# Optimization experiments

Measured on AMD Instinct MI355X. Metric: run time of the kernel, lower is better.

Reference implementation:

```python
import jax, jax.numpy as jnp
import numpy as np

B, T, D = 4, 1024, 2048
H = 32
HD = D // H  # 64
NEG = -1e9


def setup_inputs() -> dict:
    key = jax.random.key(0)
    ks = jax.random.split(key, 12)
    s = 0.02
    x = jax.random.normal(ks[0], (B, T, D), dtype=jnp.float32)
    # additive causal mask [1, 1, T, T]
    causal = jnp.tril(jnp.ones((T, T), dtype=bool))
    attention_mask = jnp.where(causal, 0.0, NEG).astype(jnp.float32)[None, None]
    cache = jnp.zeros((B, 2, T, H, HD), dtype=jnp.float32)
    return {
        "x": x,
        "attention_mask": attention_mask,
        "cache": cache,
        "cache_update_index": 0,
        "Wq": jax.random.normal(ks[1], (D, D), jnp.float32) * s,
        "bq": jnp.zeros((D,), jnp.float32),
        "Wk": jax.random.normal(ks[2], (D, D), jnp.float32) * s,
        "bk": jnp.zeros((D,), jnp.float32),
        "Wv": jax.random.normal(ks[3], (D, D), jnp.float32) * s,
        "bv": jnp.zeros((D,), jnp.float32),
        "Wo": jax.random.normal(ks[4], (D, D), jnp.float32) * s,
        "bo": jnp.zeros((D,), jnp.float32),
    }


def _split_heads(t):
    b, s, _ = t.shape
    return t.reshape(b, s, H, HD).transpose(0, 2, 1, 3)  # (B,H,T,HD)


def reference(x, attention_mask, cache, cache_update_index, Wq, bq, Wk, bk, Wv, bv, Wo, bo):
    q = _split_heads(x @ Wq + bq)  # (B,H,T,HD)
    k = _split_heads(x @ Wk + bk)
    v = _split_heads(x @ Wv + bv)

    # update KV cache (cache layout: [B, 2, max_len, H, HD])
    k_for_cache = k.transpose(0, 2, 1, 3)  # (B,T,H,HD)
    v_for_cache = v.transpose(0, 2, 1, 3)
    idx = (0, cache_update_index, 0, 0)
    k_cache = jax.lax.dynamic_update_slice(cache[:, 0], k_for_cache, idx)
    v_cache = jax.lax.dynamic_update_slice(cache[:, 1], v_for_cache, idx)
    new_cache = jnp.stack([k_cache, v_cache], axis=1)
    k = k_cache.transpose(0, 2, 1, 3)  # (B,H,S,HD)
    v = v_cache.transpose(0, 2, 1, 3)

    scale = jnp.asarray(HD, q.dtype) ** -0.5
    scores = jnp.einsum("bhqd,bhkd->bhqk", q, k) * scale + attention_mask.astype(q.dtype)
    attn = jax.nn.softmax(scores, axis=-1)
    ctx = jnp.einsum("bhqk,bhkd->bhqd", attn, v)  # (B,H,T,HD)
    merged = ctx.transpose(0, 2, 1, 3).reshape(x.shape[0], x.shape[1], D)
    out = merged @ Wo + bo
    return out, new_cache
```

## Files before the change

kernel.cpp:

```cpp
#include <hip/hip_runtime.h>
#include <hip/hip_bf16.h>
#include <stdint.h>


typedef __hip_bfloat16 bf16;
typedef unsigned short us;
typedef short s16x8 __attribute__((ext_vector_type(8)));
typedef float f32x4 __attribute__((ext_vector_type(4)));

#define T_SEQ   1024
#define D_MODEL 2048

__device__ inline us f2b(float f) {
    bf16 h = __float2bfloat16(f);
    return *(us*)&h;
}

typedef __attribute__((address_space(1))) const void gas_void;
typedef __attribute__((address_space(3))) void las_void;

__device__ inline void gl2lds16(const void* g, void* l) {
    __builtin_amdgcn_global_load_lds((gas_void*)g, (las_void*)l, 16, 0, 0);
}

__global__ __launch_bounds__(256)
void cvtx_kernel(const float* __restrict__ x, us* __restrict__ xb)
{
    const size_t i = ((size_t)blockIdx.x * 256 + threadIdx.x) * 8;
    float4 a = *(const float4*)(x + i);
    float4 b = *(const float4*)(x + i + 4);
    union { uint4 u; us s[8]; } p;
    p.s[0] = f2b(a.x); p.s[1] = f2b(a.y); p.s[2] = f2b(a.z); p.s[3] = f2b(a.w);
    p.s[4] = f2b(b.x); p.s[5] = f2b(b.y); p.s[6] = f2b(b.z); p.s[7] = f2b(b.w);
    *(uint4*)(xb + i) = p.u;
}

__global__ __launch_bounds__(256)
void wtrans_kernel(const float* __restrict__ W0, const float* __restrict__ W1,
                   const float* __restrict__ W2, us* __restrict__ Wt)
{
    __shared__ float tile[64][65];
    const int z = blockIdx.z;
    const float* W = (z == 0) ? W0 : (z == 1) ? W1 : W2;
    us* dst = Wt + (size_t)z * D_MODEL * D_MODEL;

    const int tid = threadIdx.x;
    const int k0 = blockIdx.y * 64, n0 = blockIdx.x * 64;

    const int rr = tid >> 4, cc = (tid & 15) * 4;
    #pragma unroll
    for (int i = 0; i < 4; ++i) {
        float4 v = *(const float4*)(W + (size_t)(k0 + rr + i * 16) * D_MODEL + n0 + cc);
        tile[rr + i * 16][cc]     = v.x;
        tile[rr + i * 16][cc + 1] = v.y;
        tile[rr + i * 16][cc + 2] = v.z;
        tile[rr + i * 16][cc + 3] = v.w;
    }
    __syncthreads();

    const int nr = tid >> 3, kc = (tid & 7) * 8;
    #pragma unroll
    for (int i = 0; i < 2; ++i) {
        const int n = nr + i * 32;
        union { uint4 u; us s[8]; } p;
        #pragma unroll
        for (int j = 0; j < 8; ++j) p.s[j] = f2b(tile[kc + j][n]);
        *(uint4*)(dst + (size_t)(n0 + n) * D_MODEL + k0 + kc) = p.u;
    }
}

__global__ __launch_bounds__(256)
void v2t_kernel(const float* __restrict__ cache, us* __restrict__ vbt)
{
    __shared__ float tile[64][65];
    const int t0 = blockIdx.x * 64;
    const int h  = blockIdx.y;
    const int b  = blockIdx.z;

    const float* src = cache + ((size_t)(b * 2 + 1) * T_SEQ) * D_MODEL + h * 64;

    const int tid = threadIdx.x;
    const int rr = tid >> 4, cc = (tid & 15) * 4;
    #pragma unroll
    for (int i = 0; i < 4; ++i) {
        float4 v = *(const float4*)(src + (size_t)(t0 + rr + i * 16) * D_MODEL + cc);
        tile[rr + i * 16][cc]     = v.x;
        tile[rr + i * 16][cc + 1] = v.y;
        tile[rr + i * 16][cc + 2] = v.z;
        tile[rr + i * 16][cc + 3] = v.w;
    }
    __syncthreads();

    const int dr = tid >> 3, tc = (tid & 7) * 8;
    #pragma unroll
    for (int i = 0; i < 2; ++i) {
        const int d = dr + i * 32;
        union { uint4 u; us s[8]; } p;
        #pragma unroll
        for (int j = 0; j < 8; ++j) p.s[j] = f2b(tile[tc + j][d]);
        *(uint4*)(vbt + (size_t)((b * 32 + h) * 64 + d) * 1024 + t0 + tc) = p.u;
    }
}

template<int MODE>
__global__ __launch_bounds__(256, 3)
void gemm128_kernel(const us* __restrict__ A, const us* __restrict__ Bt,
                    const float* __restrict__ b0, const float* __restrict__ b1,
                    const float* __restrict__ b2,
                    float* __restrict__ out0, float* __restrict__ out1,
                    const int* __restrict__ idxp)
{
    __shared__ __align__(16) us As[128 * 64];
    __shared__ __align__(16) us Bs[128 * 64];

    const int tid  = threadIdx.x;
    const int wv   = tid >> 6;
    const int lane = tid & 63;
    const int quad = lane >> 4;
    const int l15  = lane & 15;
    const int wm   = wv >> 1;
    const int wn   = wv & 1;

    const int gx  = gridDim.x;
    const int nwg = gx * gridDim.y;
    int bid = blockIdx.y * gx + blockIdx.x;
    bid = (bid & 7) * (nwg >> 3) + (bid >> 3);
    const int m0 = (bid / gx) * 128;
    const int n0 = (bid % gx) * 128;

    const int srow = lane >> 3;
    const int scol = ((lane & 7) ^ srow) * 8;
    const us* aG = A  + (size_t)(m0 + wv * 32 + srow) * D_MODEL + scol;
    const us* bG = Bt + (size_t)(n0 + wv * 32 + srow) * D_MODEL + scol;
    us* aL = As + wv * 32 * 64;
    us* bL = Bs + wv * 32 * 64;

    f32x4 acc[4][4];
    #pragma unroll
    for (int mi = 0; mi < 4; ++mi)
        #pragma unroll
        for (int ni = 0; ni < 4; ++ni) acc[mi][ni] = f32x4{0.f, 0.f, 0.f, 0.f};

    const int xr = l15 & 7;
    #define LDA(MI, KK) (*(const s16x8*)(As + (wm * 64 + (MI) * 16 + l15) * 64 \
                          + ((((KK) * 4 + quad) ^ xr) * 8)))
    #define LDB(NI, KK) (*(const s16x8*)(Bs + (wn * 64 + (NI) * 16 + l15) * 64 \
                          + ((((KK) * 4 + quad) ^ xr) * 8)))

    for (int k0 = 0; k0 < D_MODEL; k0 += 64) {
        #pragma unroll
        for (int g = 0; g < 4; ++g) {
            gl2lds16(aG + k0 + g * 8 * D_MODEL, aL + g * 512);
            gl2lds16(bG + k0 + g * 8 * D_MODEL, bL + g * 512);
        }
        __syncthreads();

        #pragma unroll
        for (int kk = 0; kk < 2; ++kk) {
            s16x8 af[4], bfr[4];
            #pragma unroll
            for (int mi = 0; mi < 4; ++mi) af[mi] = LDA(mi, kk);
            #pragma unroll
            for (int ni = 0; ni < 4; ++ni) bfr[ni] = LDB(ni, kk);
            #pragma unroll
            for (int mi = 0; mi < 4; ++mi)
                #pragma unroll
                for (int ni = 0; ni < 4; ++ni)
                    acc[mi][ni] = __builtin_amdgcn_mfma_f32_16x16x32_bf16(
                        af[mi], bfr[ni], acc[mi][ni], 0, 0, 0);
        }
        __syncthreads();
    }
    #undef LDA
    #undef LDB

    const int seg = (MODE == 3) ? (n0 >> 11) : 0;
    const float* bias = (MODE == 3) ? (seg == 0 ? b0 : (seg == 1 ? b1 : b2)) : b0;
    const int idx = (MODE == 3 && seg > 0) ? idxp[0] : 0;

    #pragma unroll
    for (int ni = 0; ni < 4; ++ni) {
        const int col = n0 + wn * 64 + ni * 16 + l15;
        const int cl  = col & (D_MODEL - 1);
        const float bv = bias[cl];
        #pragma unroll
        for (int mi = 0; mi < 4; ++mi) {
            #pragma unroll
            for (int r = 0; r < 4; ++r) {
                const int m = m0 + wm * 64 + mi * 16 + quad * 4 + r;
                const float v = acc[mi][ni][r] + bv;
                if (MODE == 0) {
                    out0[(size_t)m * D_MODEL + cl] = v;
                } else {
                    if (seg == 0) {
                        ((us*)out0)[(size_t)m * D_MODEL + cl] = f2b(v * 0.125f);
                    } else {
                        const int b  = m >> 10;
                        const int tt = ((m & 1023) + idx) & 1023;
                        out1[((size_t)(b * 2 + (seg - 1)) * T_SEQ + tt) * D_MODEL + cl] = v;
                    }
                }
            }
        }
    }
}

#define LDW 72

__global__ __launch_bounds__(512, 4)
void attn_mfma_kernel(const us* __restrict__ q, const float* __restrict__ cache,
                      const us* __restrict__ vbt, us* __restrict__ ctx)
{
    __shared__ __align__(16) us Qs[128 * LDW];
    __shared__ __align__(16) us Ks[2][64 * LDW];
    __shared__ __align__(16) us Vt[2][64 * 64];

    const int tid  = threadIdx.x;
    const int wave = tid >> 6;
    const int lane = tid & 63;
    const int quad = lane >> 4;
    const int l15  = lane & 15;
    const int xr   = l15 & 7;

    const int bh = blockIdx.x;
    const int b  = bh >> 5;
    const int h  = bh & 31;
    const int qt = 7 - blockIdx.y;

    const float* kbase = cache + ((size_t)(b * 2 + 0) * T_SEQ) * D_MODEL + h * 64;
    const us* vb_bh = vbt + (size_t)((b * 32 + h) * 64) * 1024;

    {
        const int qrow = tid >> 2;
        const int qp   = tid & 3;
        const uint4* qg = (const uint4*)(q + (size_t)(b * T_SEQ + qt * 128 + qrow) * D_MODEL
                                           + h * 64 + qp * 16);
        uint4 q0 = qg[0], q1 = qg[1];
        *(uint4*)(Qs + qrow * LDW + qp * 16)     = q0;
        *(uint4*)(Qs + qrow * LDW + qp * 16 + 8) = q1;
    }

    const int ksrow = tid >> 3;
    const int kp8   = tid & 7;
    const int vrow  = lane >> 3;
    const int vchk  = (lane & 7) ^ vrow;
    const us* vG = vb_bh + (size_t)(wave * 8 + vrow) * 1024 + vchk * 8;

    const int nkt = 2 * qt + 2;

    gl2lds16(vG, (us*)Vt[0] + wave * 512);
    {
        const float4* kg = (const float4*)(kbase + (size_t)ksrow * D_MODEL + kp8 * 8);
        float4 k0 = kg[0], k1 = kg[1];
        union { uint4 u; us s[8]; } p;
        p.s[0] = f2b(k0.x); p.s[1] = f2b(k0.y); p.s[2] = f2b(k0.z); p.s[3] = f2b(k0.w);
        p.s[4] = f2b(k1.x); p.s[5] = f2b(k1.y); p.s[6] = f2b(k1.z); p.s[7] = f2b(k1.w);
        *(uint4*)(&Ks[0][ksrow * LDW + kp8 * 8]) = p.u;
    }
    __syncthreads();

    const s16x8 qf0 = *(const s16x8*)(Qs + (wave * 16 + l15) * LDW + quad * 8);
    const s16x8 qf1 = *(const s16x8*)(Qs + (wave * 16 + l15) * LDW + 32 + quad * 8);

    f32x4 oacc[4];
    #pragma unroll
    for (int t = 0; t < 4; ++t) oacc[t] = f32x4{0.f, 0.f, 0.f, 0.f};
    float m_run[4] = {-1e30f, -1e30f, -1e30f, -1e30f};
    float l_run[4] = {0.f, 0.f, 0.f, 0.f};

    for (int kt = 0; kt < nkt; ++kt) {
        const int buf = kt & 1;
        const bool more = (kt + 1 < nkt);

        float4 nk0, nk1;
        if (more) {
            gl2lds16(vG + (kt + 1) * 64, (us*)Vt[buf ^ 1] + wave * 512);
            const float4* kg = (const float4*)(kbase
                + (size_t)((kt + 1) * 64 + ksrow) * D_MODEL + kp8 * 8);
            nk0 = kg[0]; nk1 = kg[1];
        }

        const int kbr = kt * 64 - qt * 128;
        if (kbr < wave * 16 + 16) {
            const us* kb_ = Ks[buf];
            const us* vb_ = (const us*)Vt[buf];

            f32x4 sacc[4];
            #pragma unroll
            for (int t = 0; t < 4; ++t) sacc[t] = f32x4{0.f, 0.f, 0.f, 0.f};
            #pragma unroll
            for (int t = 0; t < 4; ++t) {
                s16x8 kf0 = *(const s16x8*)(kb_ + (t * 16 + l15) * LDW + quad * 8);
                s16x8 kf1 = *(const s16x8*)(kb_ + (t * 16 + l15) * LDW + 32 + quad * 8);
                sacc[t] = __builtin_amdgcn_mfma_f32_16x16x32_bf16(qf0, kf0, sacc[t], 0, 0, 0);
                sacc[t] = __builtin_amdgcn_mfma_f32_16x16x32_bf16(qf1, kf1, sacc[t], 0, 0, 0);
            }

            if (kbr + 63 > wave * 16) {
                #pragma unroll
                for (int t = 0; t < 4; ++t) {
                    const int keyl = kbr + t * 16 + l15;
                    #pragma unroll
                    for (int r = 0; r < 4; ++r) {
                        if (keyl > wave * 16 + quad * 4 + r) sacc[t][r] = -1e30f;
                    }
                }
            }

            float rmax[4];
            #pragma unroll
            for (int r = 0; r < 4; ++r)
                rmax[r] = fmaxf(fmaxf(sacc[0][r], sacc[1][r]), fmaxf(sacc[2][r], sacc[3][r]));
            #pragma unroll
            for (int off = 1; off < 16; off <<= 1) {
                #pragma unroll
                for (int r = 0; r < 4; ++r) rmax[r] = fmaxf(rmax[r], __shfl_xor(rmax[r], off, 16));
            }
            float alpha[4];
            #pragma unroll
            for (int r = 0; r < 4; ++r) {
                const float mnew = fmaxf(m_run[r], rmax[r]);
                alpha[r] = __expf(m_run[r] - mnew);
                m_run[r] = mnew;
            }
            float rsum[4] = {0.f, 0.f, 0.f, 0.f};
            #pragma unroll
            for (int t = 0; t < 4; ++t) {
                #pragma unroll
                for (int r = 0; r < 4; ++r) {
                    const float p = __expf(sacc[t][r] - m_run[r]);
                    sacc[t][r] = p;
                    rsum[r] += p;
                }
            }
            #pragma unroll
            for (int off = 1; off < 16; off <<= 1) {
                #pragma unroll
                for (int r = 0; r < 4; ++r) rsum[r] += __shfl_xor(rsum[r], off, 16);
            }
            #pragma unroll
            for (int r = 0; r < 4; ++r) l_run[r] = l_run[r] * alpha[r] + rsum[r];
            #pragma unroll
            for (int t = 0; t < 4; ++t) {
                #pragma unroll
                for (int r = 0; r < 4; ++r) oacc[t][r] *= alpha[r];
            }

            #pragma unroll
            for (int t = 0; t < 4; ++t) {
                #pragma unroll
                for (int r = 0; r < 4; ++r)
                    Qs[(wave * 16 + quad * 4 + r) * LDW + t * 16 + l15] = f2b(sacc[t][r]);
            }

            s16x8 pf0 = *(const s16x8*)(Qs + (wave * 16 + l15) * LDW + quad * 8);
            s16x8 pf1 = *(const s16x8*)(Qs + (wave * 16 + l15) * LDW + 32 + quad * 8);
            #pragma unroll
            for (int t = 0; t < 4; ++t) {
                s16x8 vf0 = *(const s16x8*)(vb_ + (t * 16 + l15) * 64 + ((quad ^ xr) * 8));
                s16x8 vf1 = *(const s16x8*)(vb_ + (t * 16 + l15) * 64 + (((4 + quad) ^ xr) * 8));
                oacc[t] = __builtin_amdgcn_mfma_f32_16x16x32_bf16(pf0, vf0, oacc[t], 0, 0, 0);
                oacc[t] = __builtin_amdgcn_mfma_f32_16x16x32_bf16(pf1, vf1, oacc[t], 0, 0, 0);
            }
        }

        if (more) {
            union { uint4 u; us s[8]; } p;
            p.s[0] = f2b(nk0.x); p.s[1] = f2b(nk0.y); p.s[2] = f2b(nk0.z); p.s[3] = f2b(nk0.w);
            p.s[4] = f2b(nk1.x); p.s[5] = f2b(nk1.y); p.s[6] = f2b(nk1.z); p.s[7] = f2b(nk1.w);
            *(uint4*)(&Ks[buf ^ 1][ksrow * LDW + kp8 * 8]) = p.u;
        }
        __syncthreads();
    }

    float invl[4];
    #pragma unroll
    for (int r = 0; r < 4; ++r) invl[r] = 1.0f / l_run[r];
    #pragma unroll
    for (int r = 0; r < 4; ++r) {
        const int qrow = qt * 128 + wave * 16 + quad * 4 + r;
        us* orow = ctx + (size_t)(b * T_SEQ + qrow) * D_MODEL + h * 64;
        #pragma unroll
        for (int t = 0; t < 4; ++t) orow[t * 16 + l15] = f2b(oacc[t][r] * invl[r]);
    }
}

extern "C" void kernel_launch(void* const* d_in, const int* in_sizes, int n_in,
                              void* d_out, int out_size, void* d_ws, size_t ws_size,
                              hipStream_t stream)
{
    const float* x    = (const float*)d_in[0];
    const int*   idxp = (const int*)d_in[3];
    const float* Wq   = (const float*)d_in[4];
    const float* bq   = (const float*)d_in[5];
    const float* Wk   = (const float*)d_in[6];
    const float* bk   = (const float*)d_in[7];
    const float* Wv   = (const float*)d_in[8];
    const float* bv   = (const float*)d_in[9];
    const float* Wo   = (const float*)d_in[10];
    const float* bo   = (const float*)d_in[11];

    float* out      = (float*)d_out;
    us*    xb       = (us*)d_out;
    us*    qb       = (us*)d_out + (size_t)8 * 1024 * 1024;
    float* cacheOut = out + (size_t)4 * T_SEQ * D_MODEL;

    us* WT3  = (us*)d_ws;
    us* vbt  = (us*)d_ws;
    us* ctxb = (us*)d_ws + (size_t)8 * 1024 * 1024;
    us* WTo  = (us*)d_ws;

    const dim3 tb(256);

    cvtx_kernel<<<dim3(4096), tb, 0, stream>>>(x, xb);
    wtrans_kernel<<<dim3(32, 32, 3), tb, 0, stream>>>(Wq, Wk, Wv, WT3);

    gemm128_kernel<3><<<dim3(48, 32), tb, 0, stream>>>(
        xb, WT3, bq, bk, bv, (float*)qb, cacheOut, idxp);

    v2t_kernel<<<dim3(16, 32, 4), tb, 0, stream>>>(cacheOut, vbt);

    attn_mfma_kernel<<<dim3(128, 8), dim3(512), 0, stream>>>(qb, cacheOut, vbt, ctxb);

    wtrans_kernel<<<dim3(32, 32, 1), tb, 0, stream>>>(Wo, Wo, Wo, WTo);

    gemm128_kernel<0><<<dim3(16, 32), tb, 0, stream>>>(
        ctxb, WTo, bo, nullptr, nullptr, out, nullptr, nullptr);
}
```

Baseline: 437.6 us.

## Enlarge GEMM tiles to 256x128 and pre-convert K cache to bf16

```diff
diff --git a/kernel.cpp b/kernel.cpp
--- a/kernel.cpp
+++ b/kernel.cpp
@@ -70,47 +70,62 @@
 }
 
 __global__ __launch_bounds__(256)
-void v2t_kernel(const float* __restrict__ cache, us* __restrict__ vbt)
+void kv2b_kernel(const float* __restrict__ cache, us* __restrict__ kb,
+                 us* __restrict__ vbt)
 {
     __shared__ float tile[64][65];
-    const int t0 = blockIdx.x * 64;
-    const int h  = blockIdx.y;
-    const int b  = blockIdx.z;
-
-    const float* src = cache + ((size_t)(b * 2 + 1) * T_SEQ) * D_MODEL + h * 64;
-
-    const int tid = threadIdx.x;
-    const int rr = tid >> 4, cc = (tid & 15) * 4;
-    #pragma unroll
-    for (int i = 0; i < 4; ++i) {
-        float4 v = *(const float4*)(src + (size_t)(t0 + rr + i * 16) * D_MODEL + cc);
-        tile[rr + i * 16][cc]     = v.x;
-        tile[rr + i * 16][cc + 1] = v.y;
-        tile[rr + i * 16][cc + 2] = v.z;
-        tile[rr + i * 16][cc + 3] = v.w;
-    }
-    __syncthreads();
-
-    const int dr = tid >> 3, tc = (tid & 7) * 8;
-    #pragma unroll
-    for (int i = 0; i < 2; ++i) {
-        const int d = dr + i * 32;
-        union { uint4 u; us s[8]; } p;
-        #pragma unroll
-        for (int j = 0; j < 8; ++j) p.s[j] = f2b(tile[tc + j][d]);
-        *(uint4*)(vbt + (size_t)((b * 32 + h) * 64 + d) * 1024 + t0 + tc) = p.u;
+    const int t0   = blockIdx.x * 64;
+    const int h    = blockIdx.y;
+    const int b    = blockIdx.z >> 1;
+    const int slot = blockIdx.z & 1;
+    const int tid  = threadIdx.x;
+
+    const float* src = cache + ((size_t)(b * 2 + slot) * T_SEQ) * D_MODEL + h * 64;
+
+    if (slot == 0) {
+        const int r = tid >> 2, c = (tid & 3) * 16;
+        const float4* s4 = (const float4*)(src + (size_t)(t0 + r) * D_MODEL + c);
+        float4 v0 = s4[0], v1 = s4[1], v2 = s4[2], v3 = s4[3];
+        const float vv[16] = {v0.x, v0.y, v0.z, v0.w, v1.x, v1.y, v1.z, v1.w,
+                              v2.x, v2.y, v2.z, v2.w, v3.x, v3.y, v3.z, v3.w};
+        union { uint4 u; us s[8]; } p0, p1;
+        #pragma unroll
+        for (int i = 0; i < 8; ++i) { p0.s[i] = f2b(vv[i]); p1.s[i] = f2b(vv[8 + i]); }
+        us* dst = kb + ((size_t)(b * 32 + h) * 1024 + t0 + r) * 64 + c;
+        *(uint4*)(dst)     = p0.u;
+        *(uint4*)(dst + 8) = p1.u;
+    } else {
+        const int rr = tid >> 4, cc = (tid & 15) * 4;
+        #pragma unroll
+        for (int i = 0; i < 4; ++i) {
+            float4 v = *(const float4*)(src + (size_t)(t0 + rr + i * 16) * D_MODEL + cc);
+            tile[rr + i * 16][cc]     = v.x;
+            tile[rr + i * 16][cc + 1] = v.y;
+            tile[rr + i * 16][cc + 2] = v.z;
+            tile[rr + i * 16][cc + 3] = v.w;
+        }
+        __syncthreads();
+        const int dr = tid >> 3, tc = (tid & 7) * 8;
+        #pragma unroll
+        for (int i = 0; i < 2; ++i) {
+            const int d = dr + i * 32;
+            union { uint4 u; us s[8]; } p;
+            #pragma unroll
+            for (int j = 0; j < 8; ++j) p.s[j] = f2b(tile[tc + j][d]);
+            *(uint4*)(vbt + (size_t)((b * 32 + h) * 64 + d) * 1024 + t0 + tc) = p.u;
+        }
     }
 }
 
 template<int MODE>
-__global__ __launch_bounds__(256, 3)
-void gemm128_kernel(const us* __restrict__ A, const us* __restrict__ Bt,
+__global__ __launch_bounds__(512, 2)
+void gemm256_kernel(const us* __restrict__ A, const us* __restrict__ Bt,
                     const float* __restrict__ b0, const float* __restrict__ b1,
                     const float* __restrict__ b2,
                     float* __restrict__ out0, float* __restrict__ out1,
                     const int* __restrict__ idxp)
 {
-    __shared__ __align__(16) us As[128 * 64];
+    __shared__ __align__(16) us As[256 * 64];
     __shared__ __align__(16) us Bs[128 * 64];
 
     const int tid  = threadIdx.x;
@@ -125,15 +140,15 @@
     const int nwg = gx * gridDim.y;
     int bid = blockIdx.y * gx + blockIdx.x;
     bid = (bid & 7) * (nwg >> 3) + (bid >> 3);
-    const int m0 = (bid / gx) * 128;
+    const int m0 = (bid / gx) * 256;
     const int n0 = (bid % gx) * 128;
 
     const int srow = lane >> 3;
     const int scol = ((lane & 7) ^ srow) * 8;
     const us* aG = A  + (size_t)(m0 + wv * 32 + srow) * D_MODEL + scol;
-    const us* bG = Bt + (size_t)(n0 + wv * 32 + srow) * D_MODEL + scol;
+    const us* bG = Bt + (size_t)(n0 + wv * 16 + srow) * D_MODEL + scol;
     us* aL = As + wv * 32 * 64;
-    us* bL = Bs + wv * 32 * 64;
+    us* bL = Bs + wv * 16 * 64;
 
     f32x4 acc[4][4];
     #pragma unroll
@@ -149,10 +164,11 @@
 
     for (int k0 = 0; k0 < D_MODEL; k0 += 64) {
         #pragma unroll
-        for (int g = 0; g < 4; ++g) {
+        for (int g = 0; g < 4; ++g)
             gl2lds16(aG + k0 + g * 8 * D_MODEL, aL + g * 512);
+        #pragma unroll
+        for (int g = 0; g < 2; ++g)
             gl2lds16(bG + k0 + g * 8 * D_MODEL, bL + g * 512);
-        }
         __syncthreads();
 
         #pragma unroll
@@ -208,11 +224,11 @@
 #define LDW 72
 
 __global__ __launch_bounds__(512, 4)
-void attn_mfma_kernel(const us* __restrict__ q, const float* __restrict__ cache,
+void attn_mfma_kernel(const us* __restrict__ q, const us* __restrict__ kb,
                       const us* __restrict__ vbt, us* __restrict__ ctx)
 {
     __shared__ __align__(16) us Qs[128 * LDW];
-    __shared__ __align__(16) us Ks[2][64 * LDW];
+    __shared__ __align__(16) us Ks[2][64 * 64];
     __shared__ __align__(16) us Vt[2][64 * 64];
 
     const int tid  = threadIdx.x;
@@ -227,8 +243,8 @@
     const int h  = bh & 31;
     const int qt = 7 - blockIdx.y;
 
-    const float* kbase = cache + ((size_t)(b * 2 + 0) * T_SEQ) * D_MODEL + h * 64;
-    const us* vb_bh = vbt + (size_t)((b * 32 + h) * 64) * 1024;
+    const us* kb_bh = kb  + (size_t)(b * 32 + h) * 65536;
+    const us* vb_bh = vbt + (size_t)(b * 32 + h) * 65536;
 
     {
         const int qrow = tid >> 2;
@@ -240,23 +256,15 @@
         *(uint4*)(Qs + qrow * LDW + qp * 16 + 8) = q1;
     }
 
-    const int ksrow = tid >> 3;
-    const int kp8   = tid & 7;
-    const int vrow  = lane >> 3;
-    const int vchk  = (lane & 7) ^ vrow;
-    const us* vG = vb_bh + (size_t)(wave * 8 + vrow) * 1024 + vchk * 8;
+    const int srow = lane >> 3;
+    const int schk = ((lane & 7) ^ srow) * 8;
+    const us* kG = kb_bh + (size_t)(wave * 8 + srow) * 64 + schk;
+    const us* vG = vb_bh + (size_t)(wave * 8 + srow) * 1024 + schk;
 
     const int nkt = 2 * qt + 2;
 
+    gl2lds16(kG, (us*)Ks[0] + wave * 512);
     gl2lds16(vG, (us*)Vt[0] + wave * 512);
-    {
-        const float4* kg = (const float4*)(kbase + (size_t)ksrow * D_MODEL + kp8 * 8);
-        float4 k0 = kg[0], k1 = kg[1];
-        union { uint4 u; us s[8]; } p;
-        p.s[0] = f2b(k0.x); p.s[1] = f2b(k0.y); p.s[2] = f2b(k0.z); p.s[3] = f2b(k0.w);
-        p.s[4] = f2b(k1.x); p.s[5] = f2b(k1.y); p.s[6] = f2b(k1.z); p.s[7] = f2b(k1.w);
-        *(uint4*)(&Ks[0][ksrow * LDW + kp8 * 8]) = p.u;
-    }
     __syncthreads();
 
     const s16x8 qf0 = *(const s16x8*)(Qs + (wave * 16 + l15) * LDW + quad * 8);
@@ -270,19 +278,15 @@
 
     for (int kt = 0; kt < nkt; ++kt) {
         const int buf = kt & 1;
-        const bool more = (kt + 1 < nkt);
-
-        float4 nk0, nk1;
-        if (more) {
-            gl2lds16(vG + (kt + 1) * 64, (us*)Vt[buf ^ 1] + wave * 512);
-            const float4* kg = (const float4*)(kbase
-                + (size_t)((kt + 1) * 64 + ksrow) * D_MODEL + kp8 * 8);
-            nk0 = kg[0]; nk1 = kg[1];
+
+        if (kt + 1 < nkt) {
+            gl2lds16(kG + (kt + 1) * 4096, (us*)Ks[buf ^ 1] + wave * 512);
+            gl2lds16(vG + (kt + 1) * 64,   (us*)Vt[buf ^ 1] + wave * 512);
         }
 
         const int kbr = kt * 64 - qt * 128;
         if (kbr < wave * 16 + 16) {
-            const us* kb_ = Ks[buf];
+            const us* kb_ = (const us*)Ks[buf];
             const us* vb_ = (const us*)Vt[buf];
 
             f32x4 sacc[4];
@@ -290,8 +294,8 @@
             for (int t = 0; t < 4; ++t) sacc[t] = f32x4{0.f, 0.f, 0.f, 0.f};
             #pragma unroll
             for (int t = 0; t < 4; ++t) {
-                s16x8 kf0 = *(const s16x8*)(kb_ + (t * 16 + l15) * LDW + quad * 8);
-                s16x8 kf1 = *(const s16x8*)(kb_ + (t * 16 + l15) * LDW + 32 + quad * 8);
+                s16x8 kf0 = *(const s16x8*)(kb_ + (t * 16 + l15) * 64 + ((quad ^ xr) * 8));
+                s16x8 kf1 = *(const s16x8*)(kb_ + (t * 16 + l15) * 64 + (((4 + quad) ^ xr) * 8));
                 sacc[t] = __builtin_amdgcn_mfma_f32_16x16x32_bf16(qf0, kf0, sacc[t], 0, 0, 0);
                 sacc[t] = __builtin_amdgcn_mfma_f32_16x16x32_bf16(qf1, kf1, sacc[t], 0, 0, 0);
             }
@@ -364,12 +368,6 @@
             }
         }
 
-        if (more) {
-            union { uint4 u; us s[8]; } p;
-            p.s[0] = f2b(nk0.x); p.s[1] = f2b(nk0.y); p.s[2] = f2b(nk0.z); p.s[3] = f2b(nk0.w);
-            p.s[4] = f2b(nk1.x); p.s[5] = f2b(nk1.y); p.s[6] = f2b(nk1.z); p.s[7] = f2b(nk1.w);
-            *(uint4*)(&Ks[buf ^ 1][ksrow * LDW + kp8 * 8]) = p.u;
-        }
         __syncthreads();
     }
 
@@ -402,11 +400,12 @@
 
     float* out      = (float*)d_out;
     us*    xb       = (us*)d_out;
+    us*    vbt      = (us*)d_out;
     us*    qb       = (us*)d_out + (size_t)8 * 1024 * 1024;
     float* cacheOut = out + (size_t)4 * T_SEQ * D_MODEL;
 
     us* WT3  = (us*)d_ws;
-    us* vbt  = (us*)d_ws;
+    us* kb   = (us*)d_ws;
     us* ctxb = (us*)d_ws + (size_t)8 * 1024 * 1024;
     us* WTo  = (us*)d_ws;
 
@@ -415,15 +414,15 @@
     cvtx_kernel<<<dim3(4096), tb, 0, stream>>>(x, xb);
     wtrans_kernel<<<dim3(32, 32, 3), tb, 0, stream>>>(Wq, Wk, Wv, WT3);
 
-    gemm128_kernel<3><<<dim3(48, 32), tb, 0, stream>>>(
+    gemm256_kernel<3><<<dim3(48, 16), dim3(512), 0, stream>>>(
         xb, WT3, bq, bk, bv, (float*)qb, cacheOut, idxp);
 
-    v2t_kernel<<<dim3(16, 32, 4), tb, 0, stream>>>(cacheOut, vbt);
-
-    attn_mfma_kernel<<<dim3(128, 8), dim3(512), 0, stream>>>(qb, cacheOut, vbt, ctxb);
+    kv2b_kernel<<<dim3(16, 32, 8), tb, 0, stream>>>(cacheOut, kb, vbt);
+
+    attn_mfma_kernel<<<dim3(128, 8), dim3(512), 0, stream>>>(qb, kb, vbt, ctxb);
 
     wtrans_kernel<<<dim3(32, 32, 1), tb, 0, stream>>>(Wo, Wo, Wo, WTo);
 
-    gemm128_kernel<0><<<dim3(16, 32), tb, 0, stream>>>(
+    gemm256_kernel<0><<<dim3(16, 16), dim3(512), 0, stream>>>(
         ctxb, WTo, bo, nullptr, nullptr, out, nullptr, nullptr);
 }
```

New measurement: 460.7 us. +5.3%, slower.

## Shrink attention query tile to 64 rows with 4-wave blocks

Applied to the files above, without the earlier changes.

```diff
diff --git a/kernel.cpp b/kernel.cpp
--- a/kernel.cpp
+++ b/kernel.cpp
@@ -207,14 +207,13 @@
 
 #define LDW 72
 
-__global__ __launch_bounds__(512, 4)
+__global__ __launch_bounds__(256, 3)
 void attn_mfma_kernel(const us* __restrict__ q, const float* __restrict__ cache,
                       const us* __restrict__ vbt, us* __restrict__ ctx)
 {
-    __shared__ __align__(16) us Qs[128 * LDW];
+    __shared__ __align__(16) us Qs[64 * LDW];
     __shared__ __align__(16) us Ks[2][64 * LDW];
     __shared__ __align__(16) us Vt[2][64 * 64];
-
     const int tid  = threadIdx.x;
     const int wave = tid >> 6;
     const int lane = tid & 63;
@@ -225,37 +224,37 @@
     const int bh = blockIdx.x;
     const int b  = bh >> 5;
     const int h  = bh & 31;
-    const int qt = 7 - blockIdx.y;
+    const int qt = 15 - blockIdx.y;
 
     const float* kbase = cache + ((size_t)(b * 2 + 0) * T_SEQ) * D_MODEL + h * 64;
-    const us* vb_bh = vbt + (size_t)((b * 32 + h) * 64) * 1024;
+    const us* vb_bh = vbt + (size_t)(b * 32 + h) * 65536;
+
+    const int ksrow = tid >> 2;
+    const int kpart = (tid & 3) * 16;
+    const int vrow  = lane >> 3;
+    const int vchk  = ((lane & 7) ^ vrow) * 8;
+    const us* vG0 = vb_bh + (size_t)(wave * 16 + vrow) * 1024 + vchk;
+    const us* vG1 = vb_bh + (size_t)(wave * 16 + 8 + vrow) * 1024 + vchk;
 
     {
-        const int qrow = tid >> 2;
-        const int qp   = tid & 3;
-        const uint4* qg = (const uint4*)(q + (size_t)(b * T_SEQ + qt * 128 + qrow) * D_MODEL
-                                           + h * 64 + qp * 16);
+        const uint4* qg = (const uint4*)(q + (size_t)(b * T_SEQ + qt * 64 + ksrow) * D_MODEL
+                                           + h * 64 + kpart);
         uint4 q0 = qg[0], q1 = qg[1];
-        *(uint4*)(Qs + qrow * LDW + qp * 16)     = q0;
-        *(uint4*)(Qs + qrow * LDW + qp * 16 + 8) = q1;
-    }
-
-    const int ksrow = tid >> 3;
-    const int kp8   = tid & 7;
-    const int vrow  = lane >> 3;
-    const int vchk  = (lane & 7) ^ vrow;
-    const us* vG = vb_bh + (size_t)(wave * 8 + vrow) * 1024 + vchk * 8;
-
-    const int nkt = 2 * qt + 2;
-
-    gl2lds16(vG, (us*)Vt[0] + wave * 512);
+        *(uint4*)(Qs + ksrow * LDW + kpart)     = q0;
+        *(uint4*)(Qs + ksrow * LDW + kpart + 8) = q1;
+    }
+    gl2lds16(vG0, (us*)Vt[0] + wave * 1024);
+    gl2lds16(vG1, (us*)Vt[0] + wave * 1024 + 512);
     {
-        const float4* kg = (const float4*)(kbase + (size_t)ksrow * D_MODEL + kp8 * 8);
-        float4 k0 = kg[0], k1 = kg[1];
-        union { uint4 u; us s[8]; } p;
-        p.s[0] = f2b(k0.x); p.s[1] = f2b(k0.y); p.s[2] = f2b(k0.z); p.s[3] = f2b(k0.w);
-        p.s[4] = f2b(k1.x); p.s[5] = f2b(k1.y); p.s[6] = f2b(k1.z); p.s[7] = f2b(k1.w);
-        *(uint4*)(&Ks[0][ksrow * LDW + kp8 * 8]) = p.u;
+        const float4* kg = (const float4*)(kbase + (size_t)ksrow * D_MODEL + kpart);
+        float4 k0 = kg[0], k1 = kg[1], k2 = kg[2], k3 = kg[3];
+        const float kv[16] = {k0.x, k0.y, k0.z, k0.w, k1.x, k1.y, k1.z, k1.w,
+                              k2.x, k2.y, k2.z, k2.w, k3.x, k3.y, k3.z, k3.w};
+        union { uint4 u; us s[8]; } p0, p1;
+        #pragma unroll
+        for (int i = 0; i < 8; ++i) { p0.s[i] = f2b(kv[i]); p1.s[i] = f2b(kv[8 + i]); }
+        *(uint4*)(&Ks[0][ksrow * LDW + kpart])     = p0.u;
+        *(uint4*)(&Ks[0][ksrow * LDW + kpart + 8]) = p1.u;
     }
     __syncthreads();
 
@@ -268,21 +267,21 @@
     float m_run[4] = {-1e30f, -1e30f, -1e30f, -1e30f};
     float l_run[4] = {0.f, 0.f, 0.f, 0.f};
 
-    for (int kt = 0; kt < nkt; ++kt) {
+    for (int kt = 0; kt <= qt; ++kt) {
         const int buf = kt & 1;
-        const bool more = (kt + 1 < nkt);
-
-        float4 nk0, nk1;
+        const bool more = (kt < qt);
+
+        float4 nk0, nk1, nk2, nk3;
         if (more) {
-            gl2lds16(vG + (kt + 1) * 64, (us*)Vt[buf ^ 1] + wave * 512);
+            gl2lds16(vG0 + (kt + 1) * 64, (us*)Vt[buf ^ 1] + wave * 1024);
+            gl2lds16(vG1 + (kt + 1) * 64, (us*)Vt[buf ^ 1] + wave * 1024 + 512);
             const float4* kg = (const float4*)(kbase
-                + (size_t)((kt + 1) * 64 + ksrow) * D_MODEL + kp8 * 8);
-            nk0 = kg[0]; nk1 = kg[1];
-        }
-
-        const int kbr = kt * 64 - qt * 128;
-        if (kbr < wave * 16 + 16) {
-            const us* kb_ = Ks[buf];
+                + (size_t)((kt + 1) * 64 + ksrow) * D_MODEL + kpart);
+            nk0 = kg[0]; nk1 = kg[1]; nk2 = kg[2]; nk3 = kg[3];
+        }
+
+        {
+            const us* kb_ = (const us*)Ks[buf];
             const us* vb_ = (const us*)Vt[buf];
 
             f32x4 sacc[4];
@@ -296,10 +295,10 @@
                 sacc[t] = __builtin_amdgcn_mfma_f32_16x16x32_bf16(qf1, kf1, sacc[t], 0, 0, 0);
             }
 
-            if (kbr + 63 > wave * 16) {
+            if (kt == qt) {
                 #pragma unroll
                 for (int t = 0; t < 4; ++t) {
-                    const int keyl = kbr + t * 16 + l15;
+                    const int keyl = t * 16 + l15;
                     #pragma unroll
                     for (int r = 0; r < 4; ++r) {
                         if (keyl > wave * 16 + quad * 4 + r) sacc[t][r] = -1e30f;
@@ -365,10 +364,13 @@
         }
 
         if (more) {
-            union { uint4 u; us s[8]; } p;
-            p.s[0] = f2b(nk0.x); p.s[1] = f2b(nk0.y); p.s[2] = f2b(nk0.z); p.s[3] = f2b(nk0.w);
-            p.s[4] = f2b(nk1.x); p.s[5] = f2b(nk1.y); p.s[6] = f2b(nk1.z); p.s[7] = f2b(nk1.w);
-            *(uint4*)(&Ks[buf ^ 1][ksrow * LDW + kp8 * 8]) = p.u;
+            const float kv[16] = {nk0.x, nk0.y, nk0.z, nk0.w, nk1.x, nk1.y, nk1.z, nk1.w,
+                                  nk2.x, nk2.y, nk2.z, nk2.w, nk3.x, nk3.y, nk3.z, nk3.w};
+            union { uint4 u; us s[8]; } p0, p1;
+            #pragma unroll
+            for (int i = 0; i < 8; ++i) { p0.s[i] = f2b(kv[i]); p1.s[i] = f2b(kv[8 + i]); }
+            *(uint4*)(&Ks[buf ^ 1][ksrow * LDW + kpart])     = p0.u;
+            *(uint4*)(&Ks[buf ^ 1][ksrow * LDW + kpart + 8]) = p1.u;
         }
         __syncthreads();
     }
@@ -378,7 +380,7 @@
     for (int r = 0; r < 4; ++r) invl[r] = 1.0f / l_run[r];
     #pragma unroll
     for (int r = 0; r < 4; ++r) {
-        const int qrow = qt * 128 + wave * 16 + quad * 4 + r;
+        const int qrow = qt * 64 + wave * 16 + quad * 4 + r;
         us* orow = ctx + (size_t)(b * T_SEQ + qrow) * D_MODEL + h * 64;
         #pragma unroll
         for (int t = 0; t < 4; ++t) orow[t * 16 + l15] = f2b(oacc[t][r] * invl[r]);
@@ -402,11 +404,11 @@
 
     float* out      = (float*)d_out;
     us*    xb       = (us*)d_out;
+    us*    vbt      = (us*)d_out;
     us*    qb       = (us*)d_out + (size_t)8 * 1024 * 1024;
     float* cacheOut = out + (size_t)4 * T_SEQ * D_MODEL;
 
     us* WT3  = (us*)d_ws;
-    us* vbt  = (us*)d_ws;
     us* ctxb = (us*)d_ws + (size_t)8 * 1024 * 1024;
     us* WTo  = (us*)d_ws;
 
@@ -420,7 +422,7 @@
 
     v2t_kernel<<<dim3(16, 32, 4), tb, 0, stream>>>(cacheOut, vbt);
 
-    attn_mfma_kernel<<<dim3(128, 8), dim3(512), 0, stream>>>(qb, cacheOut, vbt, ctxb);
+    attn_mfma_kernel<<<dim3(128, 16), tb, 0, stream>>>(qb, cacheOut, vbt, ctxb);
 
     wtrans_kernel<<<dim3(32, 32, 1), tb, 0, stream>>>(Wo, Wo, Wo, WTo);
 
```

Result: slower. 449.0 us (+2.6%).

## Use 256x256 double-buffered pipelined GEMM for fused QKV projection

Applied to the files above, without the earlier changes.

```diff
diff --git a/kernel.cpp b/kernel.cpp
--- a/kernel.cpp
+++ b/kernel.cpp
@@ -22,6 +22,8 @@
 __device__ inline void gl2lds16(const void* g, void* l) {
     __builtin_amdgcn_global_load_lds((gas_void*)g, (las_void*)l, 16, 0, 0);
 }
+
+#define VMC(n) asm volatile("s_waitcnt vmcnt(" #n ")" ::: "memory")
 
 __global__ __launch_bounds__(256)
 void cvtx_kernel(const float* __restrict__ x, us* __restrict__ xb)
@@ -103,76 +105,130 @@
 }
 
 template<int MODE>
-__global__ __launch_bounds__(256, 3)
-void gemm128_kernel(const us* __restrict__ A, const us* __restrict__ Bt,
-                    const float* __restrict__ b0, const float* __restrict__ b1,
-                    const float* __restrict__ b2,
-                    float* __restrict__ out0, float* __restrict__ out1,
-                    const int* __restrict__ idxp)
-{
-    __shared__ __align__(16) us As[128 * 64];
-    __shared__ __align__(16) us Bs[128 * 64];
+__global__ __launch_bounds__(512, 1)
+void gemm256p_kernel(const us* __restrict__ A, const us* __restrict__ Bt,
+                     const float* __restrict__ b0, const float* __restrict__ b1,
+                     const float* __restrict__ b2,
+                     float* __restrict__ out0, float* __restrict__ out1,
+                     const int* __restrict__ idxp)
+{
+    __shared__ __align__(16) us As[2 * 16384];
+    __shared__ __align__(16) us Bs[2 * 16384];
 
     const int tid  = threadIdx.x;
     const int wv   = tid >> 6;
     const int lane = tid & 63;
     const int quad = lane >> 4;
     const int l15  = lane & 15;
-    const int wm   = wv >> 1;
-    const int wn   = wv & 1;
-
-    const int gx  = gridDim.x;
-    const int nwg = gx * gridDim.y;
-    int bid = blockIdx.y * gx + blockIdx.x;
-    bid = (bid & 7) * (nwg >> 3) + (bid >> 3);
-    const int m0 = (bid / gx) * 128;
-    const int n0 = (bid % gx) * 128;
-
-    const int srow = lane >> 3;
-    const int scol = ((lane & 7) ^ srow) * 8;
-    const us* aG = A  + (size_t)(m0 + wv * 32 + srow) * D_MODEL + scol;
-    const us* bG = Bt + (size_t)(n0 + wv * 32 + srow) * D_MODEL + scol;
-    us* aL = As + wv * 32 * 64;
-    us* bL = Bs + wv * 32 * 64;
-
-    f32x4 acc[4][4];
-    #pragma unroll
-    for (int mi = 0; mi < 4; ++mi)
+    const int wm   = wv >> 2;
+    const int wn   = wv & 3;
+    const int m0   = blockIdx.y * 256;
+    const int n0   = blockIdx.x * 256;
+
+    const int srow = wv * 8 + (lane >> 3);
+    const int scol = ((lane & 7) ^ ((lane >> 3) & 7)) * 8;
+    const us* aG = A  + (size_t)(m0 + srow) * D_MODEL + scol;
+    const us* bG = Bt + (size_t)(n0 + srow) * D_MODEL + scol;
+    us* aD = As + wv * 512;
+    us* bD = Bs + wv * 512;
+
+    const int xq = l15 & 7;
+
+    f32x4 acc[8][4];
+    #pragma unroll
+    for (int mi = 0; mi < 8; ++mi)
         #pragma unroll
         for (int ni = 0; ni < 4; ++ni) acc[mi][ni] = f32x4{0.f, 0.f, 0.f, 0.f};
 
-    const int xr = l15 & 7;
-    #define LDA(MI, KK) (*(const s16x8*)(As + (wm * 64 + (MI) * 16 + l15) * 64 \
-                          + ((((KK) * 4 + quad) ^ xr) * 8)))
-    #define LDB(NI, KK) (*(const s16x8*)(Bs + (wn * 64 + (NI) * 16 + l15) * 64 \
-                          + ((((KK) * 4 + quad) ^ xr) * 8)))
-
-    for (int k0 = 0; k0 < D_MODEL; k0 += 64) {
-        #pragma unroll
-        for (int g = 0; g < 4; ++g) {
-            gl2lds16(aG + k0 + g * 8 * D_MODEL, aL + g * 512);
-            gl2lds16(bG + k0 + g * 8 * D_MODEL, bL + g * 512);
-        }
-        __syncthreads();
-
-        #pragma unroll
-        for (int kk = 0; kk < 2; ++kk) {
-            s16x8 af[4], bfr[4];
-            #pragma unroll
-            for (int mi = 0; mi < 4; ++mi) af[mi] = LDA(mi, kk);
-            #pragma unroll
-            for (int ni = 0; ni < 4; ++ni) bfr[ni] = LDB(ni, kk);
-            #pragma unroll
-            for (int mi = 0; mi < 4; ++mi)
-                #pragma unroll
-                for (int ni = 0; ni < 4; ++ni)
-                    acc[mi][ni] = __builtin_amdgcn_mfma_f32_16x16x32_bf16(
-                        af[mi], bfr[ni], acc[mi][ni], 0, 0, 0);
-        }
-        __syncthreads();
-    }
-    #undef LDA
-    #undef LDB
+    #define LDA(BUF, MI, KK) \
+        (*(const s16x8*)(As + (BUF)*16384 + (wm*2 + ((MI)>>2))*4096 \
+            + (((MI)&3)*16 + l15)*64 + ((((KK)*4 + quad) ^ xq) * 8)))
+    #define LDB(BUF, NI, KK) \
+        (*(const s16x8*)(Bs + (BUF)*16384 + wn*4096 \
+            + ((NI)*16 + l15)*64 + ((((KK)*4 + quad) ^ xq) * 8)))
+
+    #define STAGE_B01(NB, KOF) { gl2lds16(bG + (KOF),               bD + (NB)*16384);          \
+                                 gl2lds16(bG + (KOF) +  64*D_MODEL, bD + (NB)*16384 + 4096); }
+    #define STAGE_B23(NB, KOF) { gl2lds16(bG + (KOF) + 128*D_MODEL, bD + (NB)*16384 + 8192);  \
+                                 gl2lds16(bG + (KOF) + 192*D_MODEL, bD + (NB)*16384 + 12288); }
+    #define STAGE_A02(NB, KOF) { gl2lds16(aG + (KOF),               aD + (NB)*16384);          \
+                                 gl2lds16(aG + (KOF) + 128*D_MODEL, aD + (NB)*16384 + 8192); }
+    #define STAGE_A13(NB, KOF) { gl2lds16(aG + (KOF) +  64*D_MODEL, aD + (NB)*16384 + 4096);  \
+                                 gl2lds16(aG + (KOF) + 192*D_MODEL, aD + (NB)*16384 + 12288); }
+
+    STAGE_B01(0, 0); STAGE_B23(0, 0); STAGE_A02(0, 0); STAGE_A13(0, 0);
+    VMC(2);
+    __builtin_amdgcn_s_barrier();
+
+    #define KTILE(BUF, STG, KOFN, VM2STMT, VM4STMT) do {                          \
+        s16x8 aL[4][2], aH[4][2], bF0[2][2], bF1[2][2];                           \
+                                                          \
+        _Pragma("unroll") for (int mi = 0; mi < 4; ++mi)                          \
+            _Pragma("unroll") for (int kk = 0; kk < 2; ++kk)                      \
+                aL[mi][kk] = LDA(BUF, mi, kk);                                    \
+        _Pragma("unroll") for (int ni = 0; ni < 2; ++ni)                          \
+            _Pragma("unroll") for (int kk = 0; kk < 2; ++kk)                      \
+                bF0[ni][kk] = LDB(BUF, ni, kk);                                   \
+        if (STG) STAGE_B01((BUF)^1, KOFN);                                        \
+        __builtin_amdgcn_s_barrier();                                             \
+        __builtin_amdgcn_s_setprio(1);                                            \
+        _Pragma("unroll") for (int kk = 0; kk < 2; ++kk)                          \
+            _Pragma("unroll") for (int mi = 0; mi < 4; ++mi)                      \
+                _Pragma("unroll") for (int ni = 0; ni < 2; ++ni)                  \
+                    acc[mi][ni] = __builtin_amdgcn_mfma_f32_16x16x32_bf16(        \
+                        aL[mi][kk], bF0[ni][kk], acc[mi][ni], 0, 0, 0);           \
+        __builtin_amdgcn_s_setprio(0);                                            \
+        __builtin_amdgcn_s_barrier();                                             \
+                                                          \
+        _Pragma("unroll") for (int ni = 0; ni < 2; ++ni)                          \
+            _Pragma("unroll") for (int kk = 0; kk < 2; ++kk)                      \
+                bF1[ni][kk] = LDB(BUF, 2 + ni, kk);                               \
+        if (STG) STAGE_B23((BUF)^1, KOFN);                                        \
+        __builtin_amdgcn_s_barrier();                                             \
+        __builtin_amdgcn_s_setprio(1);                                            \
+        _Pragma("unroll") for (int kk = 0; kk < 2; ++kk)                          \
+            _Pragma("unroll") for (int mi = 0; mi < 4; ++mi)                      \
+                _Pragma("unroll") for (int ni = 0; ni < 2; ++ni)                  \
+                    acc[mi][2 + ni] = __builtin_amdgcn_mfma_f32_16x16x32_bf16(    \
+                        aL[mi][kk], bF1[ni][kk], acc[mi][2 + ni], 0, 0, 0);       \
+        __builtin_amdgcn_s_setprio(0);                                            \
+        VM2STMT;                                                                  \
+        __builtin_amdgcn_s_barrier();                                             \
+                                                          \
+        _Pragma("unroll") for (int mi = 0; mi < 4; ++mi)                          \
+            _Pragma("unroll") for (int kk = 0; kk < 2; ++kk)                      \
+                aH[mi][kk] = LDA(BUF, 4 + mi, kk);                                \
+        if (STG) STAGE_A02((BUF)^1, KOFN);                                        \
+        __builtin_amdgcn_s_barrier();                                             \
+        __builtin_amdgcn_s_setprio(1);                                            \
+        _Pragma("unroll") for (int kk = 0; kk < 2; ++kk)                          \
+            _Pragma("unroll") for (int mi = 0; mi < 4; ++mi)                      \
+                _Pragma("unroll") for (int ni = 0; ni < 2; ++ni)                  \
+                    acc[4 + mi][2 + ni] = __builtin_amdgcn_mfma_f32_16x16x32_bf16(\
+                        aH[mi][kk], bF1[ni][kk], acc[4 + mi][2 + ni], 0, 0, 0);   \
+        __builtin_amdgcn_s_setprio(0);                                            \
+        __builtin_amdgcn_s_barrier();                                             \
+                                                          \
+        if (STG) STAGE_A13((BUF)^1, KOFN);                                        \
+        __builtin_amdgcn_s_barrier();                                             \
+        __builtin_amdgcn_s_setprio(1);                                            \
+        _Pragma("unroll") for (int kk = 0; kk < 2; ++kk)                          \
+            _Pragma("unroll") for (int mi = 0; mi < 4; ++mi)                      \
+                _Pragma("unroll") for (int ni = 0; ni < 2; ++ni)                  \
+                    acc[4 + mi][ni] = __builtin_amdgcn_mfma_f32_16x16x32_bf16(    \
+                        aH[mi][kk], bF0[ni][kk], acc[4 + mi][ni], 0, 0, 0);       \
+        __builtin_amdgcn_s_setprio(0);                                            \
+        VM4STMT;                                                                  \
+        __builtin_amdgcn_s_barrier();                                             \
+    } while (0)
+
+    for (int t = 0; t < 31; ++t) {
+        const int buf = t & 1;
+        const int kofn = (t + 1) * 64;
+        if (buf == 0) KTILE(0, true, kofn, VMC(4), VMC(2));
+        else          KTILE(1, true, kofn, VMC(4), VMC(2));
+    }
+    KTILE(1, false, 0, VMC(0), VMC(0));
 
     const int seg = (MODE == 3) ? (n0 >> 11) : 0;
     const float* bias = (MODE == 3) ? (seg == 0 ? b0 : (seg == 1 ? b1 : b2)) : b0;
@@ -184,10 +240,10 @@
         const int cl  = col & (D_MODEL - 1);
         const float bv = bias[cl];
         #pragma unroll
-        for (int mi = 0; mi < 4; ++mi) {
+        for (int mi = 0; mi < 8; ++mi) {
             #pragma unroll
             for (int r = 0; r < 4; ++r) {
-                const int m = m0 + wm * 64 + mi * 16 + quad * 4 + r;
+                const int m = m0 + wm * 128 + (mi >> 2) * 64 + (mi & 3) * 16 + quad * 4 + r;
                 const float v = acc[mi][ni][r] + bv;
                 if (MODE == 0) {
                     out0[(size_t)m * D_MODEL + cl] = v;
@@ -203,11 +259,101 @@
             }
         }
     }
+    #undef LDA
+    #undef LDB
+    #undef STAGE_B01
+    #undef STAGE_B23
+    #undef STAGE_A02
+    #undef STAGE_A13
+    #undef KTILE
+}
+
+__global__ __launch_bounds__(256, 3)
+void gemm128_kernel(const us* __restrict__ A, const us* __restrict__ Bt,
+                    const float* __restrict__ b0, float* __restrict__ out0)
+{
+    __shared__ __align__(16) us As[128 * 64];
+    __shared__ __align__(16) us Bs[128 * 64];
+
+    const int tid  = threadIdx.x;
+    const int wv   = tid >> 6;
+    const int lane = tid & 63;
+    const int quad = lane >> 4;
+    const int l15  = lane & 15;
+    const int wm   = wv >> 1;
+    const int wn   = wv & 1;
+
+    const int gx  = gridDim.x;
+    const int nwg = gx * gridDim.y;
+    int bid = blockIdx.y * gx + blockIdx.x;
+    bid = (bid & 7) * (nwg >> 3) + (bid >> 3);
+    const int m0 = (bid / gx) * 128;
+    const int n0 = (bid % gx) * 128;
+
+    const int srow = lane >> 3;
+    const int scol = ((lane & 7) ^ srow) * 8;
+    const us* aG = A  + (size_t)(m0 + wv * 32 + srow) * D_MODEL + scol;
+    const us* bG = Bt + (size_t)(n0 + wv * 32 + srow) * D_MODEL + scol;
+    us* aL = As + wv * 32 * 64;
+    us* bL = Bs + wv * 32 * 64;
+
+    f32x4 acc[4][4];
+    #pragma unroll
+    for (int mi = 0; mi < 4; ++mi)
+        #pragma unroll
+        for (int ni = 0; ni < 4; ++ni) acc[mi][ni] = f32x4{0.f, 0.f, 0.f, 0.f};
+
+    const int xr = l15 & 7;
+    #define LDA(MI, KK) (*(const s16x8*)(As + (wm * 64 + (MI) * 16 + l15) * 64 \
+                          + ((((KK) * 4 + quad) ^ xr) * 8)))
+    #define LDB(NI, KK) (*(const s16x8*)(Bs + (wn * 64 + (NI) * 16 + l15) * 64 \
+                          + ((((KK) * 4 + quad) ^ xr) * 8)))
+
+    for (int k0 = 0; k0 < D_MODEL; k0 += 64) {
+        #pragma unroll
+        for (int g = 0; g < 4; ++g) {
+            gl2lds16(aG + k0 + g * 8 * D_MODEL, aL + g * 512);
+            gl2lds16(bG + k0 + g * 8 * D_MODEL, bL + g * 512);
+        }
+        __syncthreads();
+
+        #pragma unroll
+        for (int kk = 0; kk < 2; ++kk) {
+            s16x8 af[4], bfr[4];
+            #pragma unroll
+            for (int mi = 0; mi < 4; ++mi) af[mi] = LDA(mi, kk);
+            #pragma unroll
+            for (int ni = 0; ni < 4; ++ni) bfr[ni] = LDB(ni, kk);
+            #pragma unroll
+            for (int mi = 0; mi < 4; ++mi)
+                #pragma unroll
+                for (int ni = 0; ni < 4; ++ni)
+                    acc[mi][ni] = __builtin_amdgcn_mfma_f32_16x16x32_bf16(
+                        af[mi], bfr[ni], acc[mi][ni], 0, 0, 0);
+        }
+        __syncthreads();
+    }
+    #undef LDA
+    #undef LDB
+
+    #pragma unroll
+    for (int ni = 0; ni < 4; ++ni) {
+        const int cl = n0 + wn * 64 + ni * 16 + l15;
+        const float bv = b0[cl];
+        #pragma unroll
+        for (int mi = 0; mi < 4; ++mi) {
+            #pragma unroll
+            for (int r = 0; r < 4; ++r) {
+                const int m = m0 + wm * 64 + mi * 16 + quad * 4 + r;
+                out0[(size_t)m * D_MODEL + cl] = acc[mi][ni][r] + bv;
+            }
+        }
+    }
 }
 
 #define LDW 72
 
-__global__ __launch_bounds__(512, 4)
+__global__ __launch_bounds__(512)
 void attn_mfma_kernel(const us* __restrict__ q, const float* __restrict__ cache,
                       const us* __restrict__ vbt, us* __restrict__ ctx)
 {
@@ -228,7 +374,7 @@
     const int qt = 7 - blockIdx.y;
 
     const float* kbase = cache + ((size_t)(b * 2 + 0) * T_SEQ) * D_MODEL + h * 64;
-    const us* vb_bh = vbt + (size_t)((b * 32 + h) * 64) * 1024;
+    const us* vb_bh = vbt + (size_t)(b * 32 + h) * 65536;
 
     {
         const int qrow = tid >> 2;
@@ -402,11 +548,11 @@
 
     float* out      = (float*)d_out;
     us*    xb       = (us*)d_out;
+    us*    vbt      = (us*)d_out;
     us*    qb       = (us*)d_out + (size_t)8 * 1024 * 1024;
     float* cacheOut = out + (size_t)4 * T_SEQ * D_MODEL;
 
     us* WT3  = (us*)d_ws;
-    us* vbt  = (us*)d_ws;
     us* ctxb = (us*)d_ws + (size_t)8 * 1024 * 1024;
     us* WTo  = (us*)d_ws;
 
@@ -415,7 +561,7 @@
     cvtx_kernel<<<dim3(4096), tb, 0, stream>>>(x, xb);
     wtrans_kernel<<<dim3(32, 32, 3), tb, 0, stream>>>(Wq, Wk, Wv, WT3);
 
-    gemm128_kernel<3><<<dim3(48, 32), tb, 0, stream>>>(
+    gemm256p_kernel<3><<<dim3(24, 16), dim3(512), 0, stream>>>(
         xb, WT3, bq, bk, bv, (float*)qb, cacheOut, idxp);
 
     v2t_kernel<<<dim3(16, 32, 4), tb, 0, stream>>>(cacheOut, vbt);
@@ -424,6 +570,5 @@
 
     wtrans_kernel<<<dim3(32, 32, 1), tb, 0, stream>>>(Wo, Wo, Wo, WTo);
 
-    gemm128_kernel<0><<<dim3(16, 32), tb, 0, stream>>>(
-        ctxb, WTo, bo, nullptr, nullptr, out, nullptr, nullptr);
-}
+    gemm128_kernel<<<dim3(16, 32), tb, 0, stream>>>(ctxb, WTo, bo, out);
+}
```

New measurement: 1.016 ms. +132.2%, slower.
